# Performance work log

Hardware: AMD Instinct MI355X
Metric: run time of the kernel (lower is better)

Reference implementation:

```python
import jax, jax.numpy as jnp
import numpy as np

Q_DIM, V_DIM, HID = 768, 512, 512


def setup_inputs() -> dict:
    key = jax.random.key(0)
    kV, kQ, kwq, kbq, kwv, kbv = jax.random.split(key, 6)
    B, Nv, Nq = 64, 1024, 512
    V = jax.random.normal(kV, (B, Nv, V_DIM), dtype=jnp.float32)
    Q = jax.random.normal(kQ, (B, Nq, Q_DIM), dtype=jnp.float32)
    # torch Linear params: weight [out, in], bias [out]
    Wq_w = jax.random.normal(kwq, (HID, Q_DIM), dtype=jnp.float32) / np.sqrt(Q_DIM)
    Wq_b = jax.random.normal(kbq, (HID,), dtype=jnp.float32) * 0.01
    Wv_w = jax.random.normal(kwv, (HID, V_DIM), dtype=jnp.float32) / np.sqrt(V_DIM)
    Wv_b = jax.random.normal(kbv, (HID,), dtype=jnp.float32) * 0.01
    return {"V": V, "Q": Q, "Wq_w": Wq_w, "Wq_b": Wq_b, "Wv_w": Wv_w, "Wv_b": Wv_b}


def reference(V, Q, Wq_w, Wq_b, Wv_w, Wv_b):
    # Q_proj: [B, Nq, HID]; V_proj: [B, Nv, HID]
    Q_proj = jnp.einsum('bqd,hd->bqh', Q, Wq_w) + Wq_b
    V_proj = jnp.einsum('bvd,hd->bvh', V, Wv_w) + Wv_b
    # H: [B, Nq, Nv]
    H = jnp.tanh(jnp.einsum('bqh,bvh->bqv', Q_proj, V_proj))
    A_v = jax.nn.softmax(H, axis=2)              # over Nv
    V_tilde = jnp.einsum('bqv,bvd->bqd', A_v, V)  # [B, Nq, V_DIM]
    A_q = jax.nn.softmax(H, axis=1)              # softmax(H^T, dim=2) == softmax over Nq
    Q_tilde = jnp.einsum('bqv,bqd->bvd', A_q, Q)  # [B, Nv, Q_DIM]
    v_hat = V_tilde.sum(axis=1)                   # [B, V_DIM]
    q_hat = Q_tilde.sum(axis=1)                   # [B, Q_DIM]
    return (v_hat, q_hat)
```

## Files before the change

### kernel.cpp

```cpp
#include <hip/hip_runtime.h>
#include <hip/hip_bf16.h>
#include <math.h>

#define B_SZ 64
#define NQ   512
#define NV   1024
#define QD   768
#define VD   512
#define HIDD 512

typedef __bf16 bf16x8 __attribute__((ext_vector_type(8)));
typedef __bf16 bf16x4 __attribute__((ext_vector_type(4)));
typedef float  floatx4 __attribute__((ext_vector_type(4)));

__device__ __forceinline__ void g2lds16(const __bf16* g, __bf16* l) {
    __builtin_amdgcn_global_load_lds((const __attribute__((address_space(1))) void*)g,
                                     (__attribute__((address_space(3))) void*)l,
                                     16, 0, 0);
}

__device__ __forceinline__ float exptanh(float s) {
    float t = __expf(2.0f * s);
    float r = __builtin_amdgcn_rcpf(t + 1.0f);
    return __expf(1.0f - 2.0f * r);
}

__global__ __launch_bounds__(256) void cvt2_k(const float* __restrict__ s0,
                                              const float* __restrict__ s1,
                                              __bf16* __restrict__ d,
                                              int n4a, int n4tot) {
    int i = blockIdx.x * 256 + threadIdx.x;
    if (i >= n4tot) return;
    const float* s = (i < n4a) ? (s0 + (size_t)i * 4) : (s1 + (size_t)(i - n4a) * 4);
    float4 f = *(const float4*)s;
    bf16x4 o;
    o[0] = (__bf16)f.x; o[1] = (__bf16)f.y; o[2] = (__bf16)f.z; o[3] = (__bf16)f.w;
    *(bf16x4*)(d + (size_t)i * 4) = o;
}

__global__ __launch_bounds__(256, 2) void proj_k(
    const float* __restrict__ Qin, const float* __restrict__ Vin,
    const __bf16* __restrict__ Wqb, const __bf16* __restrict__ Wvb,
    const float* __restrict__ bq, const float* __restrict__ bv,
    __bf16* __restrict__ Qp, __bf16* __restrict__ Vp)
{
    __shared__ __bf16 As[2][64 * 32];
    __shared__ __bf16 Bs[2][512 * 32];
    const int nqblk = (B_SZ * NQ) / 64;
    const float* A; const __bf16* W; const float* bias; __bf16* Cout; int K, mblk;
    if ((int)blockIdx.x < nqblk) {
        A = Qin; W = Wqb; bias = bq; Cout = Qp; K = QD; mblk = blockIdx.x;
    } else {
        A = Vin; W = Wvb; bias = bv; Cout = Vp; K = VD; mblk = blockIdx.x - nqblk;
    }

    const int t = threadIdx.x, lane = t & 63, wave = t >> 6;
    const int fr = lane & 15, quad = lane >> 4;
    const int fo   = (quad ^ ((fr >> 1) & 3)) * 8;
    const int gksw = ((lane & 3) ^ ((lane >> 3) & 3)) * 8;
    const int tile_m = mblk * 64;
    const int wn = wave * 128;

    const __bf16* wsrc = W + (size_t)(wave * 16 + (lane >> 2)) * K + gksw;
    const int arow = t >> 2, aslot = t & 3;
    const float* ap = A + (size_t)(tile_m + arow) * K + aslot * 8;
    const int awoff = arow * 32 + ((aslot ^ ((arow >> 1) & 3)) * 8);

    floatx4 acc[4][8] = {};

    auto stage_w = [&](int p, int k0) {
        #pragma unroll
        for (int c = 0; c < 8; c++)
            g2lds16(wsrc + (size_t)(c * 64) * K + k0, &Bs[p][(c * 64 + wave * 16) * 32]);
    };
    auto cvt_a = [&](int p, float4 f0, float4 f1) {
        bf16x8 pk;
        pk[0] = (__bf16)f0.x; pk[1] = (__bf16)f0.y; pk[2] = (__bf16)f0.z; pk[3] = (__bf16)f0.w;
        pk[4] = (__bf16)f1.x; pk[5] = (__bf16)f1.y; pk[6] = (__bf16)f1.z; pk[7] = (__bf16)f1.w;
        *(bf16x8*)&As[p][awoff] = pk;
    };
    auto compute = [&](int p) {
        bf16x8 af[4];
        #pragma unroll
        for (int i = 0; i < 4; i++)
            af[i] = *(const bf16x8*)&As[p][(16 * i + fr) * 32 + fo];
        #pragma unroll
        for (int j = 0; j < 8; j++) {
            bf16x8 bg = *(const bf16x8*)&Bs[p][(wn + 16 * j + fr) * 32 + fo];
            #pragma unroll
            for (int i = 0; i < 4; i++)
                acc[i][j] = __builtin_amdgcn_mfma_f32_16x16x32_bf16(af[i], bg, acc[i][j], 0, 0, 0);
        }
    };

    {
        float4 f0 = *(const float4*)(ap);
        float4 f1 = *(const float4*)(ap + 4);
        stage_w(0, 0);
        cvt_a(0, f0, f1);
    }
    __syncthreads();
    int cur = 0;
    for (int k0 = 32; k0 < K; k0 += 32) {
        float4 f0 = *(const float4*)(ap + k0);
        float4 f1 = *(const float4*)(ap + k0 + 4);
        const int nxt = cur ^ 1;
        stage_w(nxt, k0);
        compute(cur);
        cvt_a(nxt, f0, f1);
        __syncthreads();
        cur = nxt;
    }
    compute(cur);

    #pragma unroll
    for (int j = 0; j < 8; j++) {
        const int col = wn + 16 * j + fr;
        const float bvv = bias[col];
        #pragma unroll
        for (int i = 0; i < 4; i++)
            #pragma unroll
            for (int r = 0; r < 4; r++) {
                const int row = tile_m + 16 * i + quad * 4 + r;
                Cout[(size_t)row * HIDD + col] = (__bf16)(acc[i][j][r] + bvv);
            }
    }
}

__global__ __launch_bounds__(256, 2) void gemm_h(
    const __bf16* __restrict__ Qp, const __bf16* __restrict__ Vp,
    __bf16* __restrict__ Eg, float* __restrict__ R, float* __restrict__ Csum)
{
    __shared__ __bf16 As[2][128 * 32];
    __shared__ __bf16 Bs[2][256 * 32];
    const int b      = blockIdx.z;
    const int tile_q = blockIdx.y * 128;
    const int tile_v = blockIdx.x * 256;
    const int t = threadIdx.x, lane = t & 63, wave = t >> 6;
    const int fr = lane & 15, quad = lane >> 4;
    const int fo   = (quad ^ ((fr >> 1) & 3)) * 8;
    const int gksw = ((lane & 3) ^ ((lane >> 3) & 3)) * 8;
    const int wm = (wave >> 1) * 64, wn = (wave & 1) * 128;

    const __bf16* Aq = Qp + ((size_t)b * NQ + tile_q + wave * 16 + (lane >> 2)) * HIDD + gksw;
    const __bf16* Bv = Vp + ((size_t)b * NV + tile_v + wave * 16 + (lane >> 2)) * HIDD + gksw;

    auto stage = [&](int p, int k0) {
        #pragma unroll
        for (int c = 0; c < 2; c++)
            g2lds16(Aq + (size_t)(c * 64) * HIDD + k0, &As[p][(c * 64 + wave * 16) * 32]);
        #pragma unroll
        for (int c = 0; c < 4; c++)
            g2lds16(Bv + (size_t)(c * 64) * HIDD + k0, &Bs[p][(c * 64 + wave * 16) * 32]);
    };

    floatx4 acc[4][8] = {};
    auto compute = [&](int p) {
        bf16x8 af[4];
        #pragma unroll
        for (int i = 0; i < 4; i++)
            af[i] = *(const bf16x8*)&As[p][(wm + 16 * i + fr) * 32 + fo];
        #pragma unroll
        for (int j = 0; j < 8; j++) {
            bf16x8 bg = *(const bf16x8*)&Bs[p][(wn + 16 * j + fr) * 32 + fo];
            #pragma unroll
            for (int i = 0; i < 4; i++)
                acc[i][j] = __builtin_amdgcn_mfma_f32_16x16x32_bf16(af[i], bg, acc[i][j], 0, 0, 0);
        }
    };

    stage(0, 0);
    __syncthreads();
    int cur = 0;
    for (int k0 = 32; k0 < HIDD; k0 += 32) {
        stage(cur ^ 1, k0);
        compute(cur);
        __syncthreads();
        cur ^= 1;
    }
    compute(cur);

    #pragma unroll
    for (int i = 0; i < 4; i++)
        #pragma unroll
        for (int j = 0; j < 8; j++)
            #pragma unroll
            for (int r = 0; r < 4; r++)
                acc[i][j][r] = exptanh(acc[i][j][r]);

    #pragma unroll
    for (int i = 0; i < 4; i++)
        #pragma unroll
        for (int r = 0; r < 4; r++) {
            const size_t rowbase =
                ((size_t)b * NQ + tile_q + wm + 16 * i + quad * 4 + r) * NV + tile_v;
            #pragma unroll
            for (int j = 0; j < 8; j++)
                Eg[rowbase + wn + 16 * j + fr] = (__bf16)acc[i][j][r];
        }

    #pragma unroll
    for (int i = 0; i < 4; i++)
        #pragma unroll
        for (int r = 0; r < 4; r++) {
            float s = 0.f;
            #pragma unroll
            for (int j = 0; j < 8; j++) s += acc[i][j][r];
            s += __shfl_xor(s, 1); s += __shfl_xor(s, 2);
            s += __shfl_xor(s, 4); s += __shfl_xor(s, 8);
            if (fr == 0)
                atomicAdd(&R[b * NQ + tile_q + wm + 16 * i + quad * 4 + r], s);
        }
    #pragma unroll
    for (int j = 0; j < 8; j++) {
        float s = 0.f;
        #pragma unroll
        for (int i = 0; i < 4; i++)
            #pragma unroll
            for (int r = 0; r < 4; r++) s += acc[i][j][r];
        s += __shfl_xor(s, 16); s += __shfl_xor(s, 32);
        if (quad == 0)
            atomicAdd(&Csum[b * NV + tile_v + wn + 16 * j + fr], s);
    }
}

__global__ __launch_bounds__(512) void marg_k(
    const __bf16* __restrict__ E, const float* __restrict__ R,
    const float* __restrict__ C, float* __restrict__ sv,
    float* __restrict__ sq)
{
    __shared__ float sred[8][1024];
    const int b  = blockIdx.y;
    const int q0 = blockIdx.x * 64;
    const int t = threadIdx.x, lane = t & 63, wave = t >> 6;
    const float* Cb = C + b * NV;
    float ci[2][8];
    float svp[2][8] = {};
    #pragma unroll
    for (int c = 0; c < 2; c++) {
        float4 c0 = *(const float4*)&Cb[c * 512 + lane * 8];
        float4 c1 = *(const float4*)&Cb[c * 512 + lane * 8 + 4];
        ci[c][0] = 1.0f / c0.x; ci[c][1] = 1.0f / c0.y;
        ci[c][2] = 1.0f / c0.z; ci[c][3] = 1.0f / c0.w;
        ci[c][4] = 1.0f / c1.x; ci[c][5] = 1.0f / c1.y;
        ci[c][6] = 1.0f / c1.z; ci[c][7] = 1.0f / c1.w;
    }
    const float* Rb = R + b * NQ + q0 + wave * 8;
    const __bf16* Ebase = E + ((size_t)b * NQ + q0 + wave * 8) * NV;
    #pragma unroll
    for (int rr = 0; rr < 8; rr++) {
        const __bf16* Erow = Ebase + (size_t)rr * NV;
        const float ri = 1.0f / Rb[rr];
        float p = 0.f;
        #pragma unroll
        for (int c = 0; c < 2; c++) {
            bf16x8 ev = *(const bf16x8*)&Erow[c * 512 + lane * 8];
            #pragma unroll
            for (int k = 0; k < 8; k++) {
                float e = (float)ev[k];
                svp[c][k] += e * ri;
                p += e * ci[c][k];
            }
        }
        p += __shfl_xor(p, 1);  p += __shfl_xor(p, 2);  p += __shfl_xor(p, 4);
        p += __shfl_xor(p, 8);  p += __shfl_xor(p, 16); p += __shfl_xor(p, 32);
        if (lane == 0) sq[b * NQ + q0 + wave * 8 + rr] = p;
    }
    #pragma unroll
    for (int c = 0; c < 2; c++) {
        float4 w0 = { svp[c][0], svp[c][1], svp[c][2], svp[c][3] };
        float4 w1 = { svp[c][4], svp[c][5], svp[c][6], svp[c][7] };
        *(float4*)&sred[wave][c * 512 + lane * 8]     = w0;
        *(float4*)&sred[wave][c * 512 + lane * 8 + 4] = w1;
    }
    __syncthreads();
    const int v = t * 2;
    float s0 = 0.f, s1 = 0.f;
    #pragma unroll
    for (int w = 0; w < 8; w++) { s0 += sred[w][v]; s1 += sred[w][v + 1]; }
    atomicAdd(&sv[b * NV + v],     s0);
    atomicAdd(&sv[b * NV + v + 1], s1);
}

__global__ __launch_bounds__(512) void vhat_k(const float* __restrict__ sv,
                                              const float* __restrict__ V,
                                              float* __restrict__ vh_part) {
    __shared__ float svl[256];
    __shared__ float4 red[4][128];
    const int b  = blockIdx.y;
    const int v0 = blockIdx.x * 256;
    const int t  = threadIdx.x;
    if (t < 256) svl[t] = sv[b * NV + v0 + t];
    __syncthreads();
    const int g = t >> 7, gi = t & 127;
    const float* Vb = V + ((size_t)b * NV + v0 + g) * VD + gi * 4;
    float4 a = {0.f, 0.f, 0.f, 0.f};
    #pragma unroll 8
    for (int i = 0; i < 64; i++) {
        const float s = svl[g + 4 * i];
        const float4 x = *(const float4*)(Vb + (size_t)(4 * i) * VD);
        a.x += s * x.x; a.y += s * x.y; a.z += s * x.z; a.w += s * x.w;
    }
    red[g][gi] = a;
    __syncthreads();
    if (t < 128) {
        float4 r0 = red[0][t], r1 = red[1][t], r2 = red[2][t], r3 = red[3][t];
        float4 o;
        o.x = r0.x + r1.x + r2.x + r3.x;
        o.y = r0.y + r1.y + r2.y + r3.y;
        o.z = r0.z + r1.z + r2.z + r3.z;
        o.w = r0.w + r1.w + r2.w + r3.w;
        *(float4*)&vh_part[((size_t)blockIdx.x * B_SZ + b) * VD + t * 4] = o;
    }
}

__global__ __launch_bounds__(384) void qhat_k(const float* __restrict__ sq,
                                              const float* __restrict__ Q,
                                              float* __restrict__ qh_part) {
    __shared__ float sql[128];
    __shared__ float4 red[2][192];
    const int b  = blockIdx.y;
    const int q0 = blockIdx.x * 128;
    const int t  = threadIdx.x;
    if (t < 128) sql[t] = sq[b * NQ + q0 + t];
    __syncthreads();
    const int g = (t >= 192) ? 1 : 0, gi = t - g * 192;
    const float* Qb = Q + ((size_t)b * NQ + q0 + g) * QD + gi * 4;
    float4 a = {0.f, 0.f, 0.f, 0.f};
    #pragma unroll 8
    for (int i = 0; i < 64; i++) {
        const float s = sql[g + 2 * i];
        const float4 x = *(const float4*)(Qb + (size_t)(2 * i) * QD);
        a.x += s * x.x; a.y += s * x.y; a.z += s * x.z; a.w += s * x.w;
    }
    red[g][gi] = a;
    __syncthreads();
    if (t < 192) {
        float4 r0 = red[0][t], r1 = red[1][t];
        float4 o;
        o.x = r0.x + r1.x; o.y = r0.y + r1.y;
        o.z = r0.z + r1.z; o.w = r0.w + r1.w;
        *(float4*)&qh_part[((size_t)blockIdx.x * B_SZ + b) * QD + t * 4] = o;
    }
}

__global__ __launch_bounds__(256) void fin_k(const float* __restrict__ vh_part,
                                             const float* __restrict__ qh_part,
                                             float* __restrict__ out) {
    const int i = blockIdx.x * 256 + threadIdx.x;
    const int nv = B_SZ * VD;
    const int nq = B_SZ * QD;
    if (i < nv) {
        float s = 0.f;
        #pragma unroll
        for (int p = 0; p < 4; p++) s += vh_part[(size_t)p * nv + i];
        out[i] = s;
    } else if (i < nv + nq) {
        const int j = i - nv;
        float s = 0.f;
        #pragma unroll
        for (int p = 0; p < 4; p++) s += qh_part[(size_t)p * nq + j];
        out[i] = s;
    }
}

extern "C" void kernel_launch(void* const* d_in, const int* in_sizes, int n_in,
                              void* d_out, int out_size, void* d_ws, size_t ws_size,
                              hipStream_t stream) {
    const float* V    = (const float*)d_in[0];
    const float* Q    = (const float*)d_in[1];
    const float* Wq_w = (const float*)d_in[2];
    const float* Wq_b = (const float*)d_in[3];
    const float* Wv_w = (const float*)d_in[4];
    const float* Wv_b = (const float*)d_in[5];
    float* out = (float*)d_out;

    const size_t nQp = (size_t)B_SZ * NQ * HIDD;
    const size_t nVp = (size_t)B_SZ * NV * HIDD;
    const size_t nE  = (size_t)B_SZ * NQ * NV;
    const size_t nWq = (size_t)HIDD * QD;
    const size_t nWv = (size_t)HIDD * VD;
    __bf16* Qp = (__bf16*)d_ws;
    __bf16* Vp = Qp + nQp;
    __bf16* E  = Vp + nVp;
    float* R   = (float*)(E + nE);
    float* C   = R + (size_t)B_SZ * NQ;
    float* sv  = C + (size_t)B_SZ * NV;
    float* sq  = sv + (size_t)B_SZ * NV;
    __bf16* Wq = (__bf16*)(sq + (size_t)B_SZ * NQ);
    __bf16* Wv = Wq + nWq;
    float* vh_part = (float*)Wq;
    float* qh_part = vh_part + (size_t)4 * B_SZ * VD;
    size_t need = (nQp + nVp + nE + nWq + nWv) * 2 +
                  ((size_t)B_SZ * (NQ + NV) * 2) * 4;
    if (ws_size < need) return;

    hipMemsetAsync(R, 0, ((size_t)B_SZ * (NQ + 2 * NV)) * sizeof(float), stream);

    cvt2_k<<<(int)((nWq + nWv) / 1024), 256, 0, stream>>>(
        Wq_w, Wv_w, Wq, (int)(nWq / 4), (int)((nWq + nWv) / 4));

    proj_k<<<(B_SZ * NQ) / 64 + (B_SZ * NV) / 64, 256, 0, stream>>>(
        Q, V, Wq, Wv, Wq_b, Wv_b, Qp, Vp);

    gemm_h<<<dim3(NV / 256, NQ / 128, B_SZ), 256, 0, stream>>>(Qp, Vp, E, R, C);

    marg_k<<<dim3(NQ / 64, B_SZ), 512, 0, stream>>>(E, R, C, sv, sq);

    vhat_k<<<dim3(NV / 256, B_SZ), 512, 0, stream>>>(sv, V, vh_part);
    qhat_k<<<dim3(NQ / 128, B_SZ), 384, 0, stream>>>(sq, Q, qh_part);

    fin_k<<<(B_SZ * (VD + QD) + 255) / 256, 256, 0, stream>>>(vh_part, qh_part, out);
}
```

Before: 461.8 us.

## Pre-pack weights in swizzled LDS layout and enlarge projection tile to 128 rows

The weight conversion kernel now writes bf16 weights already laid out in the per-k-step swizzled LDS order, so the projection GEMM loads them with contiguous register loads instead of strided global-to-LDS copies. The projection kernel doubles its M tile to 128 rows with 512 threads (8 waves in a 2x4 grid), halving how often each weight tile is re-fetched per output row. It also switches to register-prefetch double buffering two steps ahead with a lighter LDS-only barrier. The cost is more registers held for prefetched data, which could limit occupancy.

```diff
diff --git a/kernel.cpp b/kernel.cpp
--- a/kernel.cpp
+++ b/kernel.cpp
@@ -25,65 +25,94 @@
     return __expf(1.0f - 2.0f * r);
 }
 
-__global__ __launch_bounds__(256) void cvt2_k(const float* __restrict__ s0,
-                                              const float* __restrict__ s1,
-                                              __bf16* __restrict__ d,
-                                              int n4a, int n4tot) {
-    int i = blockIdx.x * 256 + threadIdx.x;
-    if (i >= n4tot) return;
-    const float* s = (i < n4a) ? (s0 + (size_t)i * 4) : (s1 + (size_t)(i - n4a) * 4);
-    float4 f = *(const float4*)s;
-    bf16x4 o;
-    o[0] = (__bf16)f.x; o[1] = (__bf16)f.y; o[2] = (__bf16)f.z; o[3] = (__bf16)f.w;
-    *(bf16x4*)(d + (size_t)i * 4) = o;
-}
-
-__global__ __launch_bounds__(256, 2) void proj_k(
+__device__ __forceinline__ void lds_barrier() {
+    asm volatile("s_waitcnt lgkmcnt(0)" ::: "memory");
+    __builtin_amdgcn_sched_barrier(0);
+    __builtin_amdgcn_s_barrier();
+}
+
+__global__ __launch_bounds__(256) void cvtpack_k(const float* __restrict__ wq,
+                                                 const float* __restrict__ wv,
+                                                 __bf16* __restrict__ dq,
+                                                 __bf16* __restrict__ dv) {
+    const int i = blockIdx.x * 256 + threadIdx.x;
+    const int nq8 = (HIDD * QD) / 8;
+    const float* W; __bf16* d; int K, o;
+    if (i < nq8) { W = wq; d = dq; K = QD; o = i * 8; }
+    else         { W = wv; d = dv; K = VD; o = (i - nq8) * 8; }
+    const int step = o >> 14;
+    const int rem  = o & 16383;
+    const int R    = rem >> 5;
+    const int qsw  = (rem >> 3) & 3;
+    const int q    = qsw ^ ((R >> 1) & 3);
+    const float* src = W + (size_t)R * K + step * 32 + q * 8;
+    float4 f0 = *(const float4*)src;
+    float4 f1 = *(const float4*)(src + 4);
+    bf16x8 pk;
+    pk[0] = (__bf16)f0.x; pk[1] = (__bf16)f0.y; pk[2] = (__bf16)f0.z; pk[3] = (__bf16)f0.w;
+    pk[4] = (__bf16)f1.x; pk[5] = (__bf16)f1.y; pk[6] = (__bf16)f1.z; pk[7] = (__bf16)f1.w;
+    *(bf16x8*)(d + o) = pk;
+}
+
+__global__ __launch_bounds__(512, 2) void proj_k(
     const float* __restrict__ Qin, const float* __restrict__ Vin,
-    const __bf16* __restrict__ Wqb, const __bf16* __restrict__ Wvb,
+    const __bf16* __restrict__ Wqpk, const __bf16* __restrict__ Wvpk,
     const float* __restrict__ bq, const float* __restrict__ bv,
     __bf16* __restrict__ Qp, __bf16* __restrict__ Vp)
 {
-    __shared__ __bf16 As[2][64 * 32];
+    __shared__ __bf16 As[2][128 * 32];
     __shared__ __bf16 Bs[2][512 * 32];
-    const int nqblk = (B_SZ * NQ) / 64;
-    const float* A; const __bf16* W; const float* bias; __bf16* Cout; int K, mblk;
+    const int nqblk = (B_SZ * NQ) / 128;
+    const float* A; const __bf16* Wpk; const float* bias; __bf16* Cout; int K, mblk;
     if ((int)blockIdx.x < nqblk) {
-        A = Qin; W = Wqb; bias = bq; Cout = Qp; K = QD; mblk = blockIdx.x;
+        A = Qin; Wpk = Wqpk; bias = bq; Cout = Qp; K = QD; mblk = blockIdx.x;
     } else {
-        A = Vin; W = Wvb; bias = bv; Cout = Vp; K = VD; mblk = blockIdx.x - nqblk;
-    }
+        A = Vin; Wpk = Wvpk; bias = bv; Cout = Vp; K = VD; mblk = blockIdx.x - nqblk;
+    }
+    const int nsteps = K / 32;
 
     const int t = threadIdx.x, lane = t & 63, wave = t >> 6;
     const int fr = lane & 15, quad = lane >> 4;
-    const int fo   = (quad ^ ((fr >> 1) & 3)) * 8;
-    const int gksw = ((lane & 3) ^ ((lane >> 3) & 3)) * 8;
-    const int tile_m = mblk * 64;
-    const int wn = wave * 128;
-
-    const __bf16* wsrc = W + (size_t)(wave * 16 + (lane >> 2)) * K + gksw;
+    const int fo = (quad ^ ((fr >> 1) & 3)) * 8;
+    const int tile_m = mblk * 128;
+    const int wm = (wave >> 2) * 64;
+    const int wn = (wave & 3) * 128;
+
     const int arow = t >> 2, aslot = t & 3;
     const float* ap = A + (size_t)(tile_m + arow) * K + aslot * 8;
     const int awoff = arow * 32 + ((aslot ^ ((arow >> 1) & 3)) * 8);
+    const __bf16* wp = Wpk + t * 8;
 
     floatx4 acc[4][8] = {};
-
-    auto stage_w = [&](int p, int k0) {
-        #pragma unroll
-        for (int c = 0; c < 8; c++)
-            g2lds16(wsrc + (size_t)(c * 64) * K + k0, &Bs[p][(c * 64 + wave * 16) * 32]);
-    };
-    auto cvt_a = [&](int p, float4 f0, float4 f1) {
+    bf16x8 wr0, wr1, wr2, wr3;
+    float4 af0, af1;
+
+    auto loadW = [&](int s) {
+        const __bf16* p = wp + (size_t)s * 16384;
+        wr0 = *(const bf16x8*)(p);
+        wr1 = *(const bf16x8*)(p + 4096);
+        wr2 = *(const bf16x8*)(p + 8192);
+        wr3 = *(const bf16x8*)(p + 12288);
+    };
+    auto loadA = [&](int s) {
+        af0 = *(const float4*)(ap + s * 32);
+        af1 = *(const float4*)(ap + s * 32 + 4);
+    };
+    auto stage = [&](int p) {
+        *(bf16x8*)&Bs[p][t * 8]         = wr0;
+        *(bf16x8*)&Bs[p][4096 + t * 8]  = wr1;
+        *(bf16x8*)&Bs[p][8192 + t * 8]  = wr2;
+        *(bf16x8*)&Bs[p][12288 + t * 8] = wr3;
         bf16x8 pk;
-        pk[0] = (__bf16)f0.x; pk[1] = (__bf16)f0.y; pk[2] = (__bf16)f0.z; pk[3] = (__bf16)f0.w;
-        pk[4] = (__bf16)f1.x; pk[5] = (__bf16)f1.y; pk[6] = (__bf16)f1.z; pk[7] = (__bf16)f1.w;
+        pk[0] = (__bf16)af0.x; pk[1] = (__bf16)af0.y; pk[2] = (__bf16)af0.z; pk[3] = (__bf16)af0.w;
+        pk[4] = (__bf16)af1.x; pk[5] = (__bf16)af1.y; pk[6] = (__bf16)af1.z; pk[7] = (__bf16)af1.w;
         *(bf16x8*)&As[p][awoff] = pk;
     };
     auto compute = [&](int p) {
         bf16x8 af[4];
         #pragma unroll
         for (int i = 0; i < 4; i++)
-            af[i] = *(const bf16x8*)&As[p][(16 * i + fr) * 32 + fo];
+            af[i] = *(const bf16x8*)&As[p][(wm + 16 * i + fr) * 32 + fo];
         #pragma unroll
         for (int j = 0; j < 8; j++) {
             bf16x8 bg = *(const bf16x8*)&Bs[p][(wn + 16 * j + fr) * 32 + fo];
@@ -93,24 +122,23 @@
         }
     };
 
-    {
-        float4 f0 = *(const float4*)(ap);
-        float4 f1 = *(const float4*)(ap + 4);
-        stage_w(0, 0);
-        cvt_a(0, f0, f1);
-    }
-    __syncthreads();
+    loadW(0); loadA(0);
+    stage(0);
+    loadW(1); loadA(1);
+    lds_barrier();
+
     int cur = 0;
-    for (int k0 = 32; k0 < K; k0 += 32) {
-        float4 f0 = *(const float4*)(ap + k0);
-        float4 f1 = *(const float4*)(ap + k0 + 4);
-        const int nxt = cur ^ 1;
-        stage_w(nxt, k0);
+    for (int s = 0; s < nsteps - 2; ++s) {
+        stage(cur ^ 1);
+        loadW(s + 2); loadA(s + 2);
         compute(cur);
-        cvt_a(nxt, f0, f1);
-        __syncthreads();
-        cur = nxt;
-    }
+        lds_barrier();
+        cur ^= 1;
+    }
+    stage(cur ^ 1);
+    compute(cur);
+    lds_barrier();
+    cur ^= 1;
     compute(cur);
 
     #pragma unroll
@@ -121,7 +149,7 @@
         for (int i = 0; i < 4; i++)
             #pragma unroll
             for (int r = 0; r < 4; r++) {
-                const int row = tile_m + 16 * i + quad * 4 + r;
+                const int row = tile_m + wm + 16 * i + quad * 4 + r;
                 Cout[(size_t)row * HIDD + col] = (__bf16)(acc[i][j][r] + bvv);
             }
     }
@@ -397,10 +425,9 @@
 
     hipMemsetAsync(R, 0, ((size_t)B_SZ * (NQ + 2 * NV)) * sizeof(float), stream);
 
-    cvt2_k<<<(int)((nWq + nWv) / 1024), 256, 0, stream>>>(
-        Wq_w, Wv_w, Wq, (int)(nWq / 4), (int)((nWq + nWv) / 4));
-
-    proj_k<<<(B_SZ * NQ) / 64 + (B_SZ * NV) / 64, 256, 0, stream>>>(
+    cvtpack_k<<<(int)((nWq + nWv) / 8 / 256), 256, 0, stream>>>(Wq_w, Wv_w, Wq, Wv);
+
+    proj_k<<<(B_SZ * NQ) / 128 + (B_SZ * NV) / 128, 512, 0, stream>>>(
         Q, V, Wq, Wv, Wq_b, Wv_b, Qp, Vp);
 
     gemm_h<<<dim3(NV / 256, NQ / 128, B_SZ), 256, 0, stream>>>(Qp, Vp, E, R, C);
```

New measurement: 446.3 us. 3.4% less time.
